# Kernel tuning notes

Measured on AMD Instinct MI355X. Metric: run time of the kernel, lower is better.

The kernel has to match this reference:

```python
import jax, jax.numpy as jnp
import numpy as np

EPS = 1e-8

def setup_inputs() -> dict:
    key = jax.random.key(0)
    k1, k2, k3, k4, k5 = jax.random.split(key, 5)
    B, S, d, H = 4, 1024, 512, 8
    hd = d // H
    x = jax.random.normal(k1, (B, S, d), dtype=jnp.float32)
    V = jax.random.normal(k2, (B, S, H, hd), dtype=jnp.float32)
    # binary biological mask [B, S, S]
    M = (jax.random.uniform(k3, (B, S, S)) > 0.5).astype(jnp.float32)
    in_proj_w = jax.random.normal(k4, (3 * d, d), dtype=jnp.float32) * 0.02
    in_proj_b = jnp.zeros((3 * d,), dtype=jnp.float32)
    out_w = jax.random.normal(k5, (d, d), dtype=jnp.float32) * 0.02
    out_b = jnp.zeros((d,), dtype=jnp.float32)
    return {"x": x, "V": V, "M": M, "in_proj_w": in_proj_w,
            "in_proj_b": in_proj_b, "out_w": out_w, "out_b": out_b}


def reference(x, V, M, in_proj_w, in_proj_b, out_w, out_b):
    B, S, d = x.shape
    H, hd = V.shape[2], V.shape[3]
    # packed QKV projection (torch MHA in_proj); V slice is computed by torch
    # but its result is discarded, so only Q,K slices influence the output.
    qkv = x @ in_proj_w.T + in_proj_b            # [B, S, 3d]
    q = qkv[..., :d].reshape(B, S, H, hd).transpose(0, 2, 1, 3)        # [B,H,S,hd]
    k = qkv[..., d:2 * d].reshape(B, S, H, hd).transpose(0, 2, 1, 3)   # [B,H,S,hd]
    scores = jnp.einsum("bhqd,bhkd->bhqk", q, k) / jnp.sqrt(jnp.float32(hd))
    A = jax.nn.softmax(scores, axis=-1)           # [B,H,S,S] per-head attn weights
    # biological mask + L1 renormalization (post-hoc, as in original)
    A_sparse = A * M[:, None, :, :]
    norm = jnp.sum(jnp.abs(A_sparse), axis=-1, keepdims=True) + EPS
    A_bar = A_sparse / norm
    # custom V: [B,S,H,hd] -> [B,H,S,hd]
    Vp = V.transpose(0, 2, 1, 3)
    out = jnp.einsum("bhqk,bhkd->bhqd", A_bar, Vp)  # [B,H,S,hd]
    out = out.transpose(0, 2, 1, 3).reshape(B, S, d)
    return out @ out_w.T + out_b
```

## Files before the change

kernel.cpp:

```cpp
#include <hip/hip_runtime.h>
#include <hip/hip_bf16.h>

#define BB 4
#define SS 1024
#define DD 512
#define HH 8
#define HD 64

typedef __attribute__((ext_vector_type(8))) short bf16x8;
typedef __attribute__((ext_vector_type(4))) float f32x4;

static __device__ __forceinline__ unsigned short f2b(float f) {
  union { float f; unsigned int u; } c; c.f = f;
  return (unsigned short)((c.u + 0x7fffu + ((c.u >> 16) & 1u)) >> 16);
}

__global__ __launch_bounds__(256) void cvt_all(
    const float* __restrict__ x, const float* __restrict__ W1,
    const float* __restrict__ Wo, unsigned short* __restrict__ xb,
    unsigned short* __restrict__ W1b, unsigned short* __restrict__ Wob) {
  const int c = blockIdx.x * 256 + threadIdx.x;
  const float* src; unsigned short* dst; size_t off;
  if (c < 262144) { src = x;  dst = xb;  off = (size_t)c * 8; }
  else if (c < 327680) { src = W1; dst = W1b; off = (size_t)(c - 262144) * 8; }
  else { src = Wo; dst = Wob; off = (size_t)(c - 327680) * 8; }
  const float4 a = *(const float4*)(src + off);
  const float4 b = *(const float4*)(src + off + 4);
  union { unsigned short s[8]; uint4 v; } o;
  o.s[0] = f2b(a.x); o.s[1] = f2b(a.y); o.s[2] = f2b(a.z); o.s[3] = f2b(a.w);
  o.s[4] = f2b(b.x); o.s[5] = f2b(b.y); o.s[6] = f2b(b.z); o.s[7] = f2b(b.w);
  *(uint4*)(dst + off) = o.v;
}

__global__ __launch_bounds__(256) void vtrans(
    const float* __restrict__ V, unsigned short* __restrict__ Vt) {
  __shared__ float Ls[64][65];
  const int tid = threadIdx.x;
  const int s0 = blockIdx.x * 64, h = blockIdx.y, b = blockIdx.z;
  {
    const int r = tid >> 2, cs = (tid & 3) * 16;
    const float* src = V + ((size_t)((b * SS + s0 + r) * HH) + h) * HD + cs;
#pragma unroll
    for (int j = 0; j < 4; j++) {
      const float4 v = *(const float4*)(src + j * 4);
      Ls[r][cs + j * 4 + 0] = v.x; Ls[r][cs + j * 4 + 1] = v.y;
      Ls[r][cs + j * 4 + 2] = v.z; Ls[r][cs + j * 4 + 3] = v.w;
    }
  }
  __syncthreads();
  {
    const int d = tid >> 2, ss = (tid & 3) * 16;
    union { unsigned short s[16]; uint4 v[2]; } o;
#pragma unroll
    for (int j = 0; j < 16; j++) o.s[j] = f2b(Ls[ss + j][d]);
    unsigned short* dst =
        Vt + ((size_t)((b * HH + h) * HD + d)) * SS + s0 + ss;
    *(uint4*)dst = o.v[0];
    *(uint4*)(dst + 8) = o.v[1];
  }
}

__global__ __launch_bounds__(256) void gemm_qk(
    const unsigned short* __restrict__ xb, const unsigned short* __restrict__ W1b,
    const float* __restrict__ bias, unsigned short* __restrict__ qkb) {
  __shared__ unsigned short As[128][40];
  __shared__ unsigned short Bs[64][40];
  const int tid = threadIdx.x;
  const int lane = tid & 63, wave = tid >> 6;
  const int l16 = lane & 15, quad = lane >> 4;
  const int row0 = blockIdx.y * 128, col0 = blockIdx.x * 64;

  f32x4 acc[2][4];
#pragma unroll
  for (int i = 0; i < 2; i++)
#pragma unroll
    for (int j = 0; j < 4; j++) acc[i][j] = (f32x4){0.f, 0.f, 0.f, 0.f};

  for (int k0 = 0; k0 < DD; k0 += 32) {
    __syncthreads();
    {
      const int r = tid >> 1, cs = (tid & 1) * 16;
      const unsigned short* s = xb + (size_t)(row0 + r) * DD + k0 + cs;
      *(uint4*)&As[r][cs] = *(const uint4*)s;
      *(uint4*)&As[r][cs + 8] = *(const uint4*)(s + 8);
    }
    {
      const int r = tid >> 2, cs = (tid & 3) * 8;
      *(uint4*)&Bs[r][cs] =
          *(const uint4*)(W1b + (size_t)(col0 + r) * DD + k0 + cs);
    }
    __syncthreads();

    const bf16x8 a0 = *(const bf16x8*)&As[wave * 32 + l16][quad * 8];
    const bf16x8 a1 = *(const bf16x8*)&As[wave * 32 + 16 + l16][quad * 8];
#pragma unroll
    for (int nt = 0; nt < 4; nt++) {
      const bf16x8 bb = *(const bf16x8*)&Bs[nt * 16 + l16][quad * 8];
      acc[0][nt] = __builtin_amdgcn_mfma_f32_16x16x32_bf16(a0, bb, acc[0][nt], 0, 0, 0);
      acc[1][nt] = __builtin_amdgcn_mfma_f32_16x16x32_bf16(a1, bb, acc[1][nt], 0, 0, 0);
    }
  }

#pragma unroll
  for (int nt = 0; nt < 4; nt++) {
    const int col = col0 + nt * 16 + l16;
    const float bv = bias[col];
#pragma unroll
    for (int mi = 0; mi < 2; mi++)
#pragma unroll
      for (int reg = 0; reg < 4; reg++) {
        const int row = row0 + wave * 32 + mi * 16 + quad * 4 + reg;
        qkb[(size_t)row * 1024 + col] = f2b(acc[mi][nt][reg] + bv);
      }
  }
}

__global__ __launch_bounds__(256) void gemm_out(
    const unsigned short* __restrict__ Ab, const unsigned short* __restrict__ Wob,
    const float* __restrict__ bias, float* __restrict__ out) {
  __shared__ unsigned short As[128][40];
  __shared__ unsigned short Bs[64][40];
  const int tid = threadIdx.x;
  const int lane = tid & 63, wave = tid >> 6;
  const int l16 = lane & 15, quad = lane >> 4;
  const int row0 = blockIdx.y * 128, col0 = blockIdx.x * 64;

  f32x4 acc[2][4];
#pragma unroll
  for (int i = 0; i < 2; i++)
#pragma unroll
    for (int j = 0; j < 4; j++) acc[i][j] = (f32x4){0.f, 0.f, 0.f, 0.f};

  for (int k0 = 0; k0 < DD; k0 += 32) {
    __syncthreads();
    {
      const int r = tid >> 1, cs = (tid & 1) * 16;
      const unsigned short* s = Ab + (size_t)(row0 + r) * DD + k0 + cs;
      *(uint4*)&As[r][cs] = *(const uint4*)s;
      *(uint4*)&As[r][cs + 8] = *(const uint4*)(s + 8);
    }
    {
      const int r = tid >> 2, cs = (tid & 3) * 8;
      *(uint4*)&Bs[r][cs] =
          *(const uint4*)(Wob + (size_t)(col0 + r) * DD + k0 + cs);
    }
    __syncthreads();

    const bf16x8 a0 = *(const bf16x8*)&As[wave * 32 + l16][quad * 8];
    const bf16x8 a1 = *(const bf16x8*)&As[wave * 32 + 16 + l16][quad * 8];
#pragma unroll
    for (int nt = 0; nt < 4; nt++) {
      const bf16x8 bb = *(const bf16x8*)&Bs[nt * 16 + l16][quad * 8];
      acc[0][nt] = __builtin_amdgcn_mfma_f32_16x16x32_bf16(a0, bb, acc[0][nt], 0, 0, 0);
      acc[1][nt] = __builtin_amdgcn_mfma_f32_16x16x32_bf16(a1, bb, acc[1][nt], 0, 0, 0);
    }
  }

#pragma unroll
  for (int nt = 0; nt < 4; nt++) {
    const int col = col0 + nt * 16 + l16;
    const float bv = bias[col];
#pragma unroll
    for (int mi = 0; mi < 2; mi++)
#pragma unroll
      for (int reg = 0; reg < 4; reg++) {
        const int row = row0 + wave * 32 + mi * 16 + quad * 4 + reg;
        out[(size_t)row * DD + col] = acc[mi][nt][reg] + bv;
      }
  }
}

__global__ __launch_bounds__(256) void flash_attn_split(
    const unsigned short* __restrict__ qkb, const unsigned short* __restrict__ Vt,
    const float* __restrict__ Mmask, float* __restrict__ Opart,
    float* __restrict__ Sms) {
  __shared__ unsigned short QP[64][72];
  __shared__ unsigned short Ks[64][72];
  __shared__ unsigned short Vs[64][72];

  const int tid = threadIdx.x;
  const int lane = tid & 63, wave = tid >> 6;
  const int l16 = lane & 15, quad = lane >> 4;
  const int q0 = blockIdx.x * 64;
  const int h = blockIdx.y & 7, sp = blockIdx.y >> 3;
  const int b = blockIdx.z;

  {
    const int r = tid >> 2, cs = (tid & 3) * 16;
    const unsigned short* s = qkb + (size_t)(b * SS + q0 + r) * 1024 + h * HD + cs;
    *(uint4*)&QP[r][cs] = *(const uint4*)s;
    *(uint4*)&QP[r][cs + 8] = *(const uint4*)(s + 8);
  }
  __syncthreads();
  const bf16x8 bQ0 = *(const bf16x8*)&QP[wave * 16 + l16][quad * 8];
  const bf16x8 bQ1 = *(const bf16x8*)&QP[wave * 16 + l16][32 + quad * 8];
  unsigned short(*Ps)[72] = (unsigned short(*)[72]) & QP[wave * 16][0];

  float Smp = 0.f;
  f32x4 O[4];
#pragma unroll
  for (int i = 0; i < 4; i++) O[i] = (f32x4){0.f, 0.f, 0.f, 0.f};

  const float* mrow = Mmask + (size_t)(b * SS + q0 + wave * 16 + l16) * SS;

  for (int kt = sp * 8; kt < sp * 8 + 8; kt++) {
    const int k0 = kt * 64;

    __syncthreads();
    {
      const int r = tid >> 2, cs = (tid & 3) * 16;
      const unsigned short* s =
          qkb + (size_t)(b * SS + k0 + r) * 1024 + DD + h * HD + cs;
      *(uint4*)&Ks[r][cs] = *(const uint4*)s;
      *(uint4*)&Ks[r][cs + 8] = *(const uint4*)(s + 8);
    }
    {
      const int d = tid >> 2, cs = (tid & 3) * 16;
      const unsigned short* s =
          Vt + ((size_t)((b * HH + h) * HD + d)) * SS + k0 + cs;
      *(uint4*)&Vs[d][cs] = *(const uint4*)s;
      *(uint4*)&Vs[d][cs + 8] = *(const uint4*)(s + 8);
    }
    __syncthreads();

#pragma unroll
    for (int t = 0; t < 4; t++) {
      const bf16x8 aK0 = *(const bf16x8*)&Ks[t * 16 + l16][quad * 8];
      const bf16x8 aK1 = *(const bf16x8*)&Ks[t * 16 + l16][32 + quad * 8];
      f32x4 a = (f32x4){0.f, 0.f, 0.f, 0.f};
      a = __builtin_amdgcn_mfma_f32_16x16x32_bf16(aK0, bQ0, a, 0, 0, 0);
      a = __builtin_amdgcn_mfma_f32_16x16x32_bf16(aK1, bQ1, a, 0, 0, 0);
      const float4 m4 = *(const float4*)(mrow + k0 + t * 16 + quad * 4);
      const float e0 = __expf(a[0] * 0.125f) * m4.x;
      const float e1 = __expf(a[1] * 0.125f) * m4.y;
      const float e2 = __expf(a[2] * 0.125f) * m4.z;
      const float e3 = __expf(a[3] * 0.125f) * m4.w;
      Smp += (e0 + e1) + (e2 + e3);
      uint2 w;
      w.x = (unsigned)f2b(e0) | ((unsigned)f2b(e1) << 16);
      w.y = (unsigned)f2b(e2) | ((unsigned)f2b(e3) << 16);
      *(uint2*)&Ps[l16][t * 16 + quad * 4] = w;
    }

    const bf16x8 aP0 = *(const bf16x8*)&Ps[l16][quad * 8];
    const bf16x8 aP1 = *(const bf16x8*)&Ps[l16][32 + quad * 8];
#pragma unroll
    for (int dt = 0; dt < 4; dt++) {
      const bf16x8 bV0 = *(const bf16x8*)&Vs[dt * 16 + l16][quad * 8];
      const bf16x8 bV1 = *(const bf16x8*)&Vs[dt * 16 + l16][32 + quad * 8];
      O[dt] = __builtin_amdgcn_mfma_f32_16x16x32_bf16(aP0, bV0, O[dt], 0, 0, 0);
      O[dt] = __builtin_amdgcn_mfma_f32_16x16x32_bf16(aP1, bV1, O[dt], 0, 0, 0);
    }
  }

  Smp += __shfl_xor(Smp, 16);
  Smp += __shfl_xor(Smp, 32);
  const size_t grow0 = (size_t)(b * HH + h) * SS + q0 + wave * 16;
  const int NR = BB * HH * SS;
  if (lane < 16) Sms[(size_t)sp * NR + grow0 + lane] = Smp;
#pragma unroll
  for (int reg = 0; reg < 4; reg++) {
    const size_t obase = ((size_t)sp * NR + grow0 + quad * 4 + reg) * HD;
#pragma unroll
    for (int dt = 0; dt < 4; dt++)
      Opart[obase + dt * 16 + l16] = O[dt][reg];
  }
}

__global__ __launch_bounds__(256) void combine(
    const float* __restrict__ Opart, const float* __restrict__ Sms,
    unsigned short* __restrict__ attnb) {
  const int idx = blockIdx.x * 256 + threadIdx.x;
  const int row = idx >> 4;
  const int d = (idx & 15) * 4;
  const int NR = BB * HH * SS;
  const float4 o0 = *(const float4*)(Opart + (size_t)row * HD + d);
  const float4 o1 = *(const float4*)(Opart + ((size_t)NR + row) * HD + d);
  const float s = Sms[row] + Sms[NR + row];
  const float inv = 1.0f / (s + 1e-12f);
  const int b = row >> 13, h = (row >> 10) & 7, q = row & 1023;
  union { unsigned short us[4]; uint2 v; } o;
  o.us[0] = f2b((o0.x + o1.x) * inv);
  o.us[1] = f2b((o0.y + o1.y) * inv);
  o.us[2] = f2b((o0.z + o1.z) * inv);
  o.us[3] = f2b((o0.w + o1.w) * inv);
  *(uint2*)(attnb + (size_t)(b * SS + q) * DD + h * HD + d) = o.v;
}

extern "C" void kernel_launch(void* const* d_in, const int* in_sizes, int n_in,
                              void* d_out, int out_size, void* d_ws,
                              size_t ws_size, hipStream_t stream) {
  const float* x = (const float*)d_in[0];
  const float* V = (const float*)d_in[1];
  const float* Mmask = (const float*)d_in[2];
  const float* in_proj_w = (const float*)d_in[3];
  const float* in_proj_b = (const float*)d_in[4];
  const float* out_w = (const float*)d_in[5];
  const float* out_b = (const float*)d_in[6];
  float* out = (float*)d_out;

  unsigned char* ws = (unsigned char*)d_ws;
  unsigned short* qkb   = (unsigned short*)(ws);
  unsigned short* xb    = (unsigned short*)(ws + (8ull << 20));
  unsigned short* W1b   = (unsigned short*)(ws + (12ull << 20));
  unsigned short* Wob   = (unsigned short*)(ws + (13ull << 20));
  unsigned short* Vt    = (unsigned short*)(ws + (14ull << 20));
  unsigned short* attnb = (unsigned short*)(ws + (18ull << 20));
  float*          Opart = (float*)(ws + (22ull << 20));
  float*          Sms   = (float*)(ws + (38ull << 20));

  cvt_all<<<1408, 256, 0, stream>>>(x, in_proj_w, out_w, xb, W1b, Wob);
  vtrans<<<dim3(SS / 64, HH, BB), 256, 0, stream>>>(V, Vt);
  gemm_qk<<<dim3(16, 32), 256, 0, stream>>>(xb, W1b, in_proj_b, qkb);
  flash_attn_split<<<dim3(SS / 64, 2 * HH, BB), 256, 0, stream>>>(
      qkb, Vt, Mmask, Opart, Sms);
  combine<<<2048, 256, 0, stream>>>(Opart, Sms, attnb);
  gemm_out<<<dim3(8, 32), 256, 0, stream>>>(attnb, Wob, out_b, out);
}
```

Baseline: 150.4 us.

## Bit-pack attention mask in merged prep kernel and shrink out-GEMM tiles

Merges the bf16 conversion and V-transpose kernels into one prep launch that also packs the float mask into a bitmask, one bit per element. The attention kernel then reads 16 bytes of mask per row per split instead of a float for each key, which cuts the mask traffic that was being read 16 times (once per head and split) roughly 32-fold. The output GEMM moves to 64-row tiles so twice as many blocks run. The cost is an extra full pass over the mask in prep. Packing with >0.5 assumes the mask is strictly binary.

```diff
diff --git a/kernel.cpp b/kernel.cpp
--- a/kernel.cpp
+++ b/kernel.cpp
@@ -15,48 +15,61 @@
   return (unsigned short)((c.u + 0x7fffu + ((c.u >> 16) & 1u)) >> 16);
 }
 
-__global__ __launch_bounds__(256) void cvt_all(
+__global__ __launch_bounds__(256) void prep(
     const float* __restrict__ x, const float* __restrict__ W1,
-    const float* __restrict__ Wo, unsigned short* __restrict__ xb,
-    unsigned short* __restrict__ W1b, unsigned short* __restrict__ Wob) {
-  const int c = blockIdx.x * 256 + threadIdx.x;
-  const float* src; unsigned short* dst; size_t off;
-  if (c < 262144) { src = x;  dst = xb;  off = (size_t)c * 8; }
-  else if (c < 327680) { src = W1; dst = W1b; off = (size_t)(c - 262144) * 8; }
-  else { src = Wo; dst = Wob; off = (size_t)(c - 327680) * 8; }
-  const float4 a = *(const float4*)(src + off);
-  const float4 b = *(const float4*)(src + off + 4);
-  union { unsigned short s[8]; uint4 v; } o;
-  o.s[0] = f2b(a.x); o.s[1] = f2b(a.y); o.s[2] = f2b(a.z); o.s[3] = f2b(a.w);
-  o.s[4] = f2b(b.x); o.s[5] = f2b(b.y); o.s[6] = f2b(b.z); o.s[7] = f2b(b.w);
-  *(uint4*)(dst + off) = o.v;
-}
-
-__global__ __launch_bounds__(256) void vtrans(
-    const float* __restrict__ V, unsigned short* __restrict__ Vt) {
+    const float* __restrict__ Wo, const float* __restrict__ Mmask,
+    const float* __restrict__ V, unsigned short* __restrict__ xb,
+    unsigned short* __restrict__ W1b, unsigned short* __restrict__ Wob,
+    unsigned char* __restrict__ Mpack, unsigned short* __restrict__ Vt) {
   __shared__ float Ls[64][65];
+  const int bid = blockIdx.x;
   const int tid = threadIdx.x;
-  const int s0 = blockIdx.x * 64, h = blockIdx.y, b = blockIdx.z;
-  {
-    const int r = tid >> 2, cs = (tid & 3) * 16;
-    const float* src = V + ((size_t)((b * SS + s0 + r) * HH) + h) * HD + cs;
-#pragma unroll
-    for (int j = 0; j < 4; j++) {
-      const float4 v = *(const float4*)(src + j * 4);
-      Ls[r][cs + j * 4 + 0] = v.x; Ls[r][cs + j * 4 + 1] = v.y;
-      Ls[r][cs + j * 4 + 2] = v.z; Ls[r][cs + j * 4 + 3] = v.w;
-    }
-  }
-  __syncthreads();
-  {
-    const int d = tid >> 2, ss = (tid & 3) * 16;
-    union { unsigned short s[16]; uint4 v[2]; } o;
-#pragma unroll
-    for (int j = 0; j < 16; j++) o.s[j] = f2b(Ls[ss + j][d]);
-    unsigned short* dst =
-        Vt + ((size_t)((b * HH + h) * HD + d)) * SS + s0 + ss;
-    *(uint4*)dst = o.v[0];
-    *(uint4*)(dst + 8) = o.v[1];
+
+  if (bid < 1408) {
+    const float* src; unsigned short* dst; size_t off;
+    if (bid < 1024) { src = x;  dst = xb;  off = ((size_t)bid * 256 + tid) * 8; }
+    else if (bid < 1280) { src = W1; dst = W1b; off = ((size_t)(bid - 1024) * 256 + tid) * 8; }
+    else { src = Wo; dst = Wob; off = ((size_t)(bid - 1280) * 256 + tid) * 8; }
+    const float4 a = *(const float4*)(src + off);
+    const float4 b = *(const float4*)(src + off + 4);
+    union { unsigned short s[8]; uint4 v; } o;
+    o.s[0] = f2b(a.x); o.s[1] = f2b(a.y); o.s[2] = f2b(a.z); o.s[3] = f2b(a.w);
+    o.s[4] = f2b(b.x); o.s[5] = f2b(b.y); o.s[6] = f2b(b.z); o.s[7] = f2b(b.w);
+    *(uint4*)(dst + off) = o.v;
+  } else if (bid < 3456) {
+    const size_t g = (size_t)(bid - 1408) * 256 + tid;
+    const float4 a = *(const float4*)(Mmask + g * 8);
+    const float4 b = *(const float4*)(Mmask + g * 8 + 4);
+    unsigned v = 0;
+    v |= (a.x > 0.5f) ? 1u : 0u;   v |= (a.y > 0.5f) ? 2u : 0u;
+    v |= (a.z > 0.5f) ? 4u : 0u;   v |= (a.w > 0.5f) ? 8u : 0u;
+    v |= (b.x > 0.5f) ? 16u : 0u;  v |= (b.y > 0.5f) ? 32u : 0u;
+    v |= (b.z > 0.5f) ? 64u : 0u;  v |= (b.w > 0.5f) ? 128u : 0u;
+    Mpack[g] = (unsigned char)v;
+  } else {
+    const int id = bid - 3456;
+    const int s0 = (id & 15) * 64, h = (id >> 4) & 7, b = id >> 7;
+    {
+      const int r = tid >> 2, cs = (tid & 3) * 16;
+      const float* src = V + ((size_t)((b * SS + s0 + r) * HH) + h) * HD + cs;
+#pragma unroll
+      for (int j = 0; j < 4; j++) {
+        const float4 v = *(const float4*)(src + j * 4);
+        Ls[r][cs + j * 4 + 0] = v.x; Ls[r][cs + j * 4 + 1] = v.y;
+        Ls[r][cs + j * 4 + 2] = v.z; Ls[r][cs + j * 4 + 3] = v.w;
+      }
+    }
+    __syncthreads();
+    {
+      const int d = tid >> 2, ss = (tid & 3) * 16;
+      union { unsigned short s[16]; uint4 v[2]; } o;
+#pragma unroll
+      for (int j = 0; j < 16; j++) o.s[j] = f2b(Ls[ss + j][d]);
+      unsigned short* dst =
+          Vt + ((size_t)((b * HH + h) * HD + d)) * SS + s0 + ss;
+      *(uint4*)dst = o.v[0];
+      *(uint4*)(dst + 8) = o.v[1];
+    }
   }
 }
 
@@ -118,41 +131,33 @@
 __global__ __launch_bounds__(256) void gemm_out(
     const unsigned short* __restrict__ Ab, const unsigned short* __restrict__ Wob,
     const float* __restrict__ bias, float* __restrict__ out) {
-  __shared__ unsigned short As[128][40];
+  __shared__ unsigned short As[64][40];
   __shared__ unsigned short Bs[64][40];
   const int tid = threadIdx.x;
   const int lane = tid & 63, wave = tid >> 6;
   const int l16 = lane & 15, quad = lane >> 4;
-  const int row0 = blockIdx.y * 128, col0 = blockIdx.x * 64;
-
-  f32x4 acc[2][4];
-#pragma unroll
-  for (int i = 0; i < 2; i++)
-#pragma unroll
-    for (int j = 0; j < 4; j++) acc[i][j] = (f32x4){0.f, 0.f, 0.f, 0.f};
+  const int row0 = blockIdx.y * 64, col0 = blockIdx.x * 64;
+
+  f32x4 acc[4];
+#pragma unroll
+  for (int j = 0; j < 4; j++) acc[j] = (f32x4){0.f, 0.f, 0.f, 0.f};
 
   for (int k0 = 0; k0 < DD; k0 += 32) {
     __syncthreads();
     {
-      const int r = tid >> 1, cs = (tid & 1) * 16;
-      const unsigned short* s = Ab + (size_t)(row0 + r) * DD + k0 + cs;
-      *(uint4*)&As[r][cs] = *(const uint4*)s;
-      *(uint4*)&As[r][cs + 8] = *(const uint4*)(s + 8);
-    }
-    {
       const int r = tid >> 2, cs = (tid & 3) * 8;
+      *(uint4*)&As[r][cs] =
+          *(const uint4*)(Ab + (size_t)(row0 + r) * DD + k0 + cs);
       *(uint4*)&Bs[r][cs] =
           *(const uint4*)(Wob + (size_t)(col0 + r) * DD + k0 + cs);
     }
     __syncthreads();
 
-    const bf16x8 a0 = *(const bf16x8*)&As[wave * 32 + l16][quad * 8];
-    const bf16x8 a1 = *(const bf16x8*)&As[wave * 32 + 16 + l16][quad * 8];
+    const bf16x8 a0 = *(const bf16x8*)&As[wave * 16 + l16][quad * 8];
 #pragma unroll
     for (int nt = 0; nt < 4; nt++) {
       const bf16x8 bb = *(const bf16x8*)&Bs[nt * 16 + l16][quad * 8];
-      acc[0][nt] = __builtin_amdgcn_mfma_f32_16x16x32_bf16(a0, bb, acc[0][nt], 0, 0, 0);
-      acc[1][nt] = __builtin_amdgcn_mfma_f32_16x16x32_bf16(a1, bb, acc[1][nt], 0, 0, 0);
+      acc[nt] = __builtin_amdgcn_mfma_f32_16x16x32_bf16(a0, bb, acc[nt], 0, 0, 0);
     }
   }
 
@@ -161,18 +166,16 @@
     const int col = col0 + nt * 16 + l16;
     const float bv = bias[col];
 #pragma unroll
-    for (int mi = 0; mi < 2; mi++)
-#pragma unroll
-      for (int reg = 0; reg < 4; reg++) {
-        const int row = row0 + wave * 32 + mi * 16 + quad * 4 + reg;
-        out[(size_t)row * DD + col] = acc[mi][nt][reg] + bv;
-      }
+    for (int reg = 0; reg < 4; reg++) {
+      const int row = row0 + wave * 16 + quad * 4 + reg;
+      out[(size_t)row * DD + col] = acc[nt][reg] + bv;
+    }
   }
 }
 
 __global__ __launch_bounds__(256) void flash_attn_split(
     const unsigned short* __restrict__ qkb, const unsigned short* __restrict__ Vt,
-    const float* __restrict__ Mmask, float* __restrict__ Opart,
+    const unsigned char* __restrict__ Mpack, float* __restrict__ Opart,
     float* __restrict__ Sms) {
   __shared__ unsigned short QP[64][72];
   __shared__ unsigned short Ks[64][72];
@@ -191,6 +194,14 @@
     *(uint4*)&QP[r][cs] = *(const uint4*)s;
     *(uint4*)&QP[r][cs + 8] = *(const uint4*)(s + 8);
   }
+
+  union { uint4 v[4]; unsigned w[16]; } mu;
+  {
+    const uint4* mp = (const uint4*)(Mpack +
+        (size_t)(b * SS + q0 + wave * 16 + l16) * 128 + sp * 64);
+    mu.v[0] = mp[0]; mu.v[1] = mp[1]; mu.v[2] = mp[2]; mu.v[3] = mp[3];
+  }
+
   __syncthreads();
   const bf16x8 bQ0 = *(const bf16x8*)&QP[wave * 16 + l16][quad * 8];
   const bf16x8 bQ1 = *(const bf16x8*)&QP[wave * 16 + l16][32 + quad * 8];
@@ -201,10 +212,10 @@
 #pragma unroll
   for (int i = 0; i < 4; i++) O[i] = (f32x4){0.f, 0.f, 0.f, 0.f};
 
-  const float* mrow = Mmask + (size_t)(b * SS + q0 + wave * 16 + l16) * SS;
-
-  for (int kt = sp * 8; kt < sp * 8 + 8; kt++) {
-    const int k0 = kt * 64;
+#pragma unroll
+  for (int i = 0; i < 8; i++) {
+    const int k0 = (sp * 8 + i) * 64;
+    const unsigned mlo = mu.w[2 * i], mhi = mu.w[2 * i + 1];
 
     __syncthreads();
     {
@@ -230,11 +241,12 @@
       f32x4 a = (f32x4){0.f, 0.f, 0.f, 0.f};
       a = __builtin_amdgcn_mfma_f32_16x16x32_bf16(aK0, bQ0, a, 0, 0, 0);
       a = __builtin_amdgcn_mfma_f32_16x16x32_bf16(aK1, bQ1, a, 0, 0, 0);
-      const float4 m4 = *(const float4*)(mrow + k0 + t * 16 + quad * 4);
-      const float e0 = __expf(a[0] * 0.125f) * m4.x;
-      const float e1 = __expf(a[1] * 0.125f) * m4.y;
-      const float e2 = __expf(a[2] * 0.125f) * m4.z;
-      const float e3 = __expf(a[3] * 0.125f) * m4.w;
+      const unsigned nib =
+          ((t < 2 ? mlo : mhi) >> ((t & 1) * 16 + quad * 4)) & 0xFu;
+      float e0 = __expf(a[0] * 0.125f); e0 = (nib & 1u) ? e0 : 0.f;
+      float e1 = __expf(a[1] * 0.125f); e1 = (nib & 2u) ? e1 : 0.f;
+      float e2 = __expf(a[2] * 0.125f); e2 = (nib & 4u) ? e2 : 0.f;
+      float e3 = __expf(a[3] * 0.125f); e3 = (nib & 8u) ? e3 : 0.f;
       Smp += (e0 + e1) + (e2 + e3);
       uint2 w;
       w.x = (unsigned)f2b(e0) | ((unsigned)f2b(e1) << 16);
@@ -308,12 +320,13 @@
   unsigned short* attnb = (unsigned short*)(ws + (18ull << 20));
   float*          Opart = (float*)(ws + (22ull << 20));
   float*          Sms   = (float*)(ws + (38ull << 20));
-
-  cvt_all<<<1408, 256, 0, stream>>>(x, in_proj_w, out_w, xb, W1b, Wob);
-  vtrans<<<dim3(SS / 64, HH, BB), 256, 0, stream>>>(V, Vt);
+  unsigned char*  Mpack = ws + (38ull << 20) + (256u << 10);
+
+  prep<<<3968, 256, 0, stream>>>(x, in_proj_w, out_w, Mmask, V,
+                                 xb, W1b, Wob, Mpack, Vt);
   gemm_qk<<<dim3(16, 32), 256, 0, stream>>>(xb, W1b, in_proj_b, qkb);
   flash_attn_split<<<dim3(SS / 64, 2 * HH, BB), 256, 0, stream>>>(
-      qkb, Vt, Mmask, Opart, Sms);
+      qkb, Vt, Mpack, Opart, Sms);
   combine<<<2048, 256, 0, stream>>>(Opart, Sms, attnb);
-  gemm_out<<<dim3(8, 32), 256, 0, stream>>>(attnb, Wob, out_b, out);
-}
+  gemm_out<<<dim3(8, 64), 256, 0, stream>>>(attnb, Wob, out_b, out);
+}
```

Result: faster. 144.2 us (-4.1%).
